# Kernel tuning notes

Hardware: AMD Instinct MI355X
Metric: run time of the kernel (lower is better)

## Reference

```python
import jax, jax.numpy as jnp
import numpy as np

HIDDEN = 2048
INTER = 4096
HEADS = 32
HEAD_DIM = INTER // HEADS  # 128
STATE = 128
GROUPS = 1
CONV_K = 4
CHUNK = 256
EPS = 1e-5
CONV_DIM = INTER + 2 * GROUPS * STATE  # 4352
DT_MIN, DT_MAX = 0.0, 100.0
BATCH, SEQ = 2, 4096


def _segment_sum(x):
    """Stable segment sum: returns (..., T, T) with entry [i,j] = sum_{k=j+1..i} x[k] (-inf above diag)."""
    T = x.shape[-1]
    xx = jnp.broadcast_to(x[..., None], x.shape + (T,))
    mask_lower = jnp.tril(jnp.ones((T, T), bool), -1)
    xx = jnp.where(mask_lower, xx, 0.0)
    seg = jnp.cumsum(xx, axis=-2)
    mask_incl = jnp.tril(jnp.ones((T, T), bool), 0)
    return jnp.where(mask_incl, seg, -jnp.inf)


def setup_inputs() -> dict:
    key = jax.random.key(0)
    ks = jax.random.split(key, 8)
    std = 0.02
    return {
        "hidden_states": jax.random.normal(ks[0], (BATCH, SEQ, HIDDEN), jnp.float32),
        "in_proj_w": jax.random.normal(ks[1], (INTER + CONV_DIM + HEADS, HIDDEN), jnp.float32) * std,
        "conv_w": jax.random.normal(ks[2], (CONV_DIM, 1, CONV_K), jnp.float32) * std,
        "conv_b": jnp.zeros((CONV_DIM,), jnp.float32),
        "A_log": jnp.log(jax.random.uniform(ks[3], (HEADS,), jnp.float32, 1.0, 16.0)),
        "dt_bias": jax.random.normal(ks[4], (HEADS,), jnp.float32) * 0.1,
        "D": jnp.ones((HEADS,), jnp.float32),
        "norm_w": jnp.ones((INTER,), jnp.float32),
        "out_proj_w": jax.random.normal(ks[5], (HIDDEN, INTER), jnp.float32) * (std / np.sqrt(48.0)),
    }


def reference(hidden_states, in_proj_w, conv_w, conv_b, A_log, dt_bias, D, norm_w, out_proj_w):
    b, s, _ = hidden_states.shape
    # in_proj and split into gate / conv-input / dt
    proj = hidden_states @ in_proj_w.T
    gate, hBC, dt = jnp.split(proj, [INTER, INTER + CONV_DIM], axis=-1)

    # causal depthwise conv1d (padding k-1 left, truncate to seq_len) + SiLU
    x = jnp.transpose(hBC, (0, 2, 1))  # (b, conv_dim, s)
    x = jax.lax.conv_general_dilated(
        x, conv_w, window_strides=(1,), padding=[(CONV_K - 1, 0)],
        dimension_numbers=("NCH", "OIH", "NCH"), feature_group_count=CONV_DIM)
    x = x + conv_b[None, :, None]
    hBC = jax.nn.silu(jnp.transpose(x, (0, 2, 1)))  # (b, s, conv_dim)

    xs, B, C = jnp.split(hBC, [INTER, INTER + GROUPS * STATE], axis=-1)

    A = -jnp.exp(A_log)  # (h,)
    dt = jnp.clip(jax.nn.softplus(dt + dt_bias), DT_MIN, DT_MAX)  # (b, s, h)

    xs = xs.reshape(b, s, HEADS, HEAD_DIM)
    rep = HEADS // GROUPS
    Bm = jnp.repeat(B.reshape(b, s, GROUPS, STATE), rep, axis=2)  # (b,s,h,n)
    Cm = jnp.repeat(C.reshape(b, s, GROUPS, STATE), rep, axis=2)

    pad = (-s) % CHUNK

    def padseq(t):
        return jnp.pad(t, ((0, 0), (0, pad)) + ((0, 0),) * (t.ndim - 2))

    D_res = D[None, None, :, None] * padseq(xs)  # (b, S, h, p)
    xdt = padseq(xs * dt[..., None])
    Ad = padseq(A[None, None, :] * dt)  # (b, S, h)
    Bm, Cm = padseq(Bm), padseq(Cm)

    nc = (s + pad) // CHUNK
    xdt = xdt.reshape(b, nc, CHUNK, HEADS, HEAD_DIM)
    Ad = jnp.transpose(Ad.reshape(b, nc, CHUNK, HEADS), (0, 3, 1, 2))  # (b,h,c,l)
    Bm = Bm.reshape(b, nc, CHUNK, HEADS, STATE)
    Cm = Cm.reshape(b, nc, CHUNK, HEADS, STATE)

    A_cum = jnp.cumsum(Ad, axis=-1)  # (b,h,c,l)

    # 1) intra-chunk (diagonal block) output
    L = jnp.exp(_segment_sum(Ad))  # (b,h,c,l,l)
    G = jnp.einsum("bclhn,bcshn->bclsh", Cm, Bm)
    M = G * jnp.transpose(L, (0, 2, 3, 4, 1))
    Y_diag = jnp.einsum("bclsh,bcshp->bclhp", M, xdt)

    # 2) per-chunk final states
    decay_states = jnp.exp(A_cum[:, :, :, -1:] - A_cum)  # (b,h,c,l)
    B_decay = Bm * jnp.transpose(decay_states, (0, 2, 3, 1))[..., None]
    states = jnp.einsum("bclhn,bclhp->bchpn", B_decay, xdt)  # (b,c,h,p,n)

    # 3) inter-chunk recurrence
    states = jnp.concatenate([jnp.zeros_like(states[:, :1]), states], axis=1)  # (b,c+1,h,p,n)
    chunk_sums = jnp.pad(A_cum[:, :, :, -1], ((0, 0), (0, 0), (1, 0)))  # (b,h,c+1)
    decay_chunk = jnp.exp(_segment_sum(chunk_sums))  # (b,h,c+1,c+1)
    decay_chunk = jnp.transpose(decay_chunk, (0, 2, 3, 1))  # (b,c,z,h)
    new_states = jnp.einsum("bczh,bchpn->bzhpn", decay_chunk, states)
    states = new_states[:, :-1]  # (b,c,h,p,n) state entering each chunk

    # 4) state -> output contribution
    state_decay = jnp.exp(A_cum)  # (b,h,c,l)
    Y_off = jnp.einsum("bclhn,bchpn->bclhp", Cm, states) * jnp.transpose(state_decay, (0, 2, 3, 1))[..., None]

    y = (Y_diag + Y_off).reshape(b, nc * CHUNK, HEADS, HEAD_DIM) + D_res
    y = y[:, :s].reshape(b, s, INTER)

    # gated RMSNorm
    y = y * jax.nn.silu(gate)
    var = jnp.mean(y * y, axis=-1, keepdims=True)
    y = y * jax.lax.rsqrt(var + EPS) * norm_w

    return y @ out_proj_w.T
```

## Files before the change

### kernel.cpp

```cpp
#include <hip/hip_runtime.h>

#define SEQ     4096
#define BATCH   2
#define NROWS   8192
#define HID     2048
#define INTER_  4096
#define NHEADS  32
#define HDIM    128
#define NSTATE  128
#define CDIM    4352
#define NPROJ_  8480
#define NPAD    8704
#define NCH     16
#define CHUNK_  256

typedef __attribute__((ext_vector_type(8))) short bf16x8;
typedef __attribute__((ext_vector_type(4))) short short4v;
typedef __attribute__((ext_vector_type(4))) float f32x4;

#define AS1 __attribute__((address_space(1)))
#define AS3 __attribute__((address_space(3)))

__device__ __forceinline__ float bf2f(short s) {
  union { unsigned u; float f; } x;
  x.u = ((unsigned)(unsigned short)s) << 16;
  return x.f;
}
__device__ __forceinline__ short f2bf(float f) {
  union { float f; unsigned u; } x; x.f = f;
  unsigned r = x.u + 0x7FFFu + ((x.u >> 16) & 1u);
  return (short)(r >> 16);
}

__global__ void cvt_bf16(const float* __restrict__ in, short* __restrict__ out,
                         int n4, int nsrc4) {
  int i = blockIdx.x * 256 + threadIdx.x;
  if (i >= n4) return;
  short4v o = {0, 0, 0, 0};
  if (i < nsrc4) {
    f32x4 v = *(const f32x4*)(in + (size_t)i * 4);
    o = (short4v){ f2bf(v.x), f2bf(v.y), f2bf(v.z), f2bf(v.w) };
  }
  *(short4v*)(out + (size_t)i * 4) = o;
}

template<int MODE>
__global__ __launch_bounds__(512, 1)
void gemm256(const short* __restrict__ A, const short* __restrict__ Bw,
             int M, int N, int K, int nM,
             float* __restrict__ outF, short* __restrict__ gate,
             short* __restrict__ hbc, float* __restrict__ dtraw)
{
  __shared__ __align__(16) short lds[2][2][2][256 * 32];
  const int tid = threadIdx.x;
  const int lane = tid & 63, wave = tid >> 6;
  const int l16 = lane & 15, lhi = lane >> 4;
  const int wm = wave >> 2, wn = wave & 3;

  const int bm = blockIdx.x % nM, bn = blockIdx.x / nM;
  const size_t row0 = (size_t)bm * 256;
  const int    col0 = bn * 256;

  const short* Ab  = A + row0 * K;
  const short* Bbp = Bw + (size_t)col0 * K;

  f32x4 acc[8][4];
  #pragma unroll
  for (int m = 0; m < 8; ++m)
    #pragma unroll
    for (int n = 0; n < 4; ++n) acc[m][n] = (f32x4){0.f, 0.f, 0.f, 0.f};

  auto stage = [&](int bufq, int mat, int kh, int ko) {
    const short* gsrc = mat ? Bbp : Ab;
    short* base = &lds[bufq][mat][kh][0];
    #pragma unroll
    for (int j = 0; j < 2; ++j) {
      int u = j * 512 + tid;
      int r = u >> 2;
      int g = (u & 3) ^ ((r >> 1) & 3);
      __builtin_amdgcn_global_load_lds(
          (const AS1 unsigned*)(gsrc + (size_t)r * K + ko + kh * 32 + g * 8),
          (AS3 unsigned*)(base + (j * 512 + wave * 64) * 8), 16, 0, 0);
    }
  };
  auto readA = [&](int bufq, int kh, int mh, bf16x8* a) {
    const short* base = &lds[bufq][0][kh][0];
    #pragma unroll
    for (int f = 0; f < 4; ++f) {
      int rr = wm * 128 + mh * 64 + f * 16 + l16;
      int g = lhi ^ ((rr >> 1) & 3);
      a[f] = *(const bf16x8*)(base + rr * 32 + g * 8);
    }
  };
  auto readB = [&](int bufq, int kh, bf16x8* b) {
    const short* base = &lds[bufq][1][kh][0];
    #pragma unroll
    for (int f = 0; f < 4; ++f) {
      int rr = wn * 64 + f * 16 + l16;
      int g = lhi ^ ((rr >> 1) & 3);
      b[f] = *(const bf16x8*)(base + rr * 32 + g * 8);
    }
  };

  const int nt = K / 64;
  stage(0, 0, 0, 0); stage(0, 1, 0, 0); stage(0, 0, 1, 0); stage(0, 1, 1, 0);
  asm volatile("s_waitcnt vmcnt(4)" ::: "memory");
  __builtin_amdgcn_s_barrier();

  for (int t = 0; t < nt; ++t) {
    const int buf = t & 1, nb = buf ^ 1;
    const int kon = (t + 1) * 64;
    const bool pf = (t + 1 < nt);

    #pragma unroll
    for (int kh = 0; kh < 2; ++kh) {
      if (pf) { stage(nb, 0, kh, kon); stage(nb, 1, kh, kon); }
      bf16x8 a[8], b[4];
      readA(buf, kh, 0, a); readA(buf, kh, 1, a + 4); readB(buf, kh, b);
      __builtin_amdgcn_s_setprio(1);
      #pragma unroll
      for (int mf = 0; mf < 8; ++mf)
        #pragma unroll
        for (int nf = 0; nf < 4; ++nf)
          acc[mf][nf] = __builtin_amdgcn_mfma_f32_16x16x32_bf16(a[mf], b[nf], acc[mf][nf], 0, 0, 0);
      __builtin_amdgcn_s_setprio(0);
      if (pf || kh == 0) {
        if (pf) asm volatile("s_waitcnt vmcnt(4)" ::: "memory");
        else    asm volatile("s_waitcnt vmcnt(0)" ::: "memory");
        __builtin_amdgcn_s_barrier();
      }
    }
  }

  #pragma unroll
  for (int mh = 0; mh < 2; ++mh) {
    #pragma unroll
    for (int f = 0; f < 4; ++f) {
      #pragma unroll
      for (int nf = 0; nf < 4; ++nf) {
        #pragma unroll
        for (int jq = 0; jq < 4; ++jq) {
          int gr = (int)row0 + wm * 128 + mh * 64 + f * 16 + lhi * 4 + jq;
          int gc = col0 + wn * 64 + nf * 16 + l16;
          float v = acc[mh * 4 + f][nf][jq];
          if (MODE == 0) {
            outF[(size_t)gr * N + gc] = v;
          } else {
            if (gc < INTER_)             gate[(size_t)gr * INTER_ + gc] = f2bf(v);
            else if (gc < INTER_ + CDIM) hbc[(size_t)gr * CDIM + (gc - INTER_)] = f2bf(v);
            else if (gc < NPROJ_)        dtraw[(size_t)gr * NHEADS + (gc - INTER_ - CDIM)] = v;
          }
        }
      }
    }
  }
}

__global__ __launch_bounds__(256)
void conv_t(const short* __restrict__ hbc, const float* __restrict__ cw,
            const float* __restrict__ cb, short* __restrict__ xsT,
            short* __restrict__ Bb, short* __restrict__ Cb, short* __restrict__ BbT)
{
  __shared__ short sOut[64][130];
  int ct = blockIdx.y;
  int cl = threadIdx.x & 127;
  int rh = threadIdx.x >> 7;
  int c = ct * 128 + cl;
  int row0 = blockIdx.x * 64;
  int s0 = row0 & (SEQ - 1);
  float w0 = cw[c * 4 + 0], w1 = cw[c * 4 + 1], w2 = cw[c * 4 + 2], w3 = cw[c * 4 + 3];
  float bias = cb[c];
  int r0 = rh * 32;
  float h0, h1, h2;
  h0 = (s0 + r0 - 3 >= 0) ? bf2f(hbc[(size_t)(row0 + r0 - 3) * CDIM + c]) : 0.f;
  h1 = (s0 + r0 - 2 >= 0) ? bf2f(hbc[(size_t)(row0 + r0 - 2) * CDIM + c]) : 0.f;
  h2 = (s0 + r0 - 1 >= 0) ? bf2f(hbc[(size_t)(row0 + r0 - 1) * CDIM + c]) : 0.f;

  for (int r = r0; r < r0 + 32; ++r) {
    float xin = bf2f(hbc[(size_t)(row0 + r) * CDIM + c]);
    float a = bias + w0 * h0 + w1 * h1 + w2 * h2 + w3 * xin;
    h0 = h1; h1 = h2; h2 = xin;
    float v = a / (1.f + expf(-a));
    short bv = f2bf(v);
    if (ct < 33) sOut[r][cl] = bv;
    if (ct == 32)      Bb[(size_t)(row0 + r) * NSTATE + cl] = bv;
    else if (ct == 33) Cb[(size_t)(row0 + r) * NSTATE + cl] = bv;
  }
  if (ct >= 33) return;
  __syncthreads();
  int p = threadIdx.x >> 1, sh = (threadIdx.x & 1) * 32;
  int b = row0 >> 12;
  size_t dst;
  short* outp;
  if (ct < 32) { outp = xsT; dst = ((size_t)(b * 32 + ct) * 128 + p) * SEQ + s0 + sh; }
  else         { outp = BbT; dst = ((size_t)b * 128 + p) * SEQ + s0 + sh; }
  #pragma unroll
  for (int g = 0; g < 8; ++g) {
    short4v o;
    o[0] = sOut[sh + g * 4 + 0][p];
    o[1] = sOut[sh + g * 4 + 1][p];
    o[2] = sOut[sh + g * 4 + 2][p];
    o[3] = sOut[sh + g * 4 + 3][p];
    *(short4v*)(outp + dst + g * 4) = o;
  }
}

__global__ void dt_proc(const float* __restrict__ dtraw, const float* __restrict__ dtb,
                        float* __restrict__ dtT, int n) {
  int i = blockIdx.x * 256 + threadIdx.x;
  if (i >= n) return;
  float x = dtraw[i] + dtb[i & (NHEADS - 1)];
  float sp = (x > 20.f) ? x : log1pf(expf(x));
  float d = fminf(fmaxf(sp, 0.f), 100.f);
  int row = i >> 5, h = i & 31;
  dtT[(size_t)h * NROWS + row] = d;
}

__global__ __launch_bounds__(256)
void ssm_state(const short* __restrict__ xsT, const short* __restrict__ BbT,
               const float* __restrict__ dtT, const float* __restrict__ Alog,
               short* __restrict__ csb, float* __restrict__ dAsum)
{
  int blk = blockIdx.x;
  int h = blk & 31, cc = (blk >> 5) & 15, b = blk >> 9;
  int tid = threadIdx.x, lane = tid & 63, wave = tid >> 6;
  int l16 = lane & 15, lhi = lane >> 4;
  int s0 = cc * CHUNK_;

  __shared__ float acum[256];
  __shared__ float sdt[256];
  __shared__ float wsum[4];
  { float Ah = -expf(Alog[h]);
    float d = dtT[(size_t)h * NROWS + (size_t)b * SEQ + s0 + tid];
    sdt[tid] = d;
    float v = Ah * d;
    #pragma unroll
    for (int off = 1; off < 64; off <<= 1) {
      float t = __shfl_up(v, off, 64);
      if (lane >= off) v += t;
    }
    if (lane == 63) wsum[wave] = v;
    __syncthreads();
    float addv = 0.f;
    #pragma unroll
    for (int w = 0; w < 3; ++w) if (w < wave) addv += wsum[w];
    acum[tid] = v + addv;
  }
  __syncthreads();
  float alast = acum[255];

  const short* xbase = xsT + ((size_t)(b * 32 + h) * 128) * SEQ + s0;
  const short* bbase = BbT + ((size_t)b * 128) * SEQ + s0;

  f32x4 acc[2][8];
  #pragma unroll
  for (int m = 0; m < 2; ++m)
    #pragma unroll
    for (int n = 0; n < 8; ++n) acc[m][n] = (f32x4){0.f, 0.f, 0.f, 0.f};

  for (int lt0 = 0; lt0 < 256; lt0 += 32) {
    float fe[8];
    #pragma unroll
    for (int e = 0; e < 8; ++e) {
      int kl = lt0 + lhi * 8 + e;
      fe[e] = sdt[kl] * __expf(alast - acum[kl]);
    }
    bf16x8 af[2];
    #pragma unroll
    for (int m = 0; m < 2; ++m) {
      bf16x8 raw = *(const bf16x8*)(xbase + (size_t)(wave * 32 + m * 16 + l16) * SEQ + lt0 + lhi * 8);
      bf16x8 sc;
      #pragma unroll
      for (int e = 0; e < 8; ++e) sc[e] = f2bf(bf2f(raw[e]) * fe[e]);
      af[m] = sc;
    }
    #pragma unroll
    for (int n = 0; n < 8; ++n) {
      bf16x8 bfv = *(const bf16x8*)(bbase + (size_t)(n * 16 + l16) * SEQ + lt0 + lhi * 8);
      acc[0][n] = __builtin_amdgcn_mfma_f32_16x16x32_bf16(af[0], bfv, acc[0][n], 0, 0, 0);
      acc[1][n] = __builtin_amdgcn_mfma_f32_16x16x32_bf16(af[1], bfv, acc[1][n], 0, 0, 0);
    }
  }
  size_t base = (size_t)blk * 16384;
  #pragma unroll
  for (int m = 0; m < 2; ++m)
    #pragma unroll
    for (int n = 0; n < 8; ++n)
      #pragma unroll
      for (int j = 0; j < 4; ++j) {
        int p = wave * 32 + m * 16 + lhi * 4 + j;
        int ng = n * 16 + l16;
        csb[base + (size_t)p * NSTATE + ng] = f2bf(acc[m][n][j]);
      }
  if (tid == 0) dAsum[blk] = alast;
}

__global__ void ssm_scan(short* __restrict__ csb, const float* __restrict__ dAsum) {
  int idx = blockIdx.x * 256 + threadIdx.x;
  int np = idx & 16383;
  int bh = idx >> 14;
  int h = bh & 31, b = bh >> 5;
  float run = 0.f;
  #pragma unroll
  for (int c = 0; c < NCH; ++c) {
    size_t base = ((size_t)((b * NCH + c) * NHEADS + h)) * 16384 + np;
    float v = bf2f(csb[base]);
    csb[base] = f2bf(run);
    run = run * __expf(dAsum[(b * NCH + c) * NHEADS + h]) + v;
  }
}

__global__ __launch_bounds__(256)
void ssm_y(const short* __restrict__ xsT, const short* __restrict__ Bb,
           const short* __restrict__ Cb, const float* __restrict__ dtT,
           const float* __restrict__ Alog, const float* __restrict__ Dv,
           const short* __restrict__ csb, short* __restrict__ gateY)
{
  int blk = blockIdx.y, lt = blockIdx.x;
  int h = blk & 31, cc = (blk >> 5) & 15, b = blk >> 9;
  int tid = threadIdx.x, lane = tid & 63, wave = tid >> 6;
  int l16 = lane & 15, lhi = lane >> 4;
  int s0 = cc * CHUNK_;
  size_t row0 = (size_t)b * SEQ + s0;

  __shared__ float acum[256];
  __shared__ float sdt[256];
  __shared__ float wsum[4];
  __shared__ __align__(16) short M_lds[64 * 264];

  { float Ah = -expf(Alog[h]);
    float d = dtT[(size_t)h * NROWS + row0 + tid];
    sdt[tid] = d;
    float v = Ah * d;
    #pragma unroll
    for (int off = 1; off < 64; off <<= 1) {
      float t = __shfl_up(v, off, 64);
      if (lane >= off) v += t;
    }
    if (lane == 63) wsum[wave] = v;
    __syncthreads();
    float addv = 0.f;
    #pragma unroll
    for (int w = 0; w < 3; ++w) if (w < wave) addv += wsum[w];
    acum[tid] = v + addv;
  }
  __syncthreads();

  float Dh = Dv[h];

  {
    f32x4 acc1[4][4];
    #pragma unroll
    for (int m = 0; m < 4; ++m)
      #pragma unroll
      for (int n = 0; n < 4; ++n) acc1[m][n] = (f32x4){0.f, 0.f, 0.f, 0.f};
    for (int kk = 0; kk < NSTATE; kk += 32) {
      bf16x8 af[4], bv[4];
      #pragma unroll
      for (int m = 0; m < 4; ++m)
        af[m] = *(const bf16x8*)(Cb + (row0 + lt * 64 + m * 16 + l16) * NSTATE + kk + lhi * 8);
      #pragma unroll
      for (int n = 0; n < 4; ++n)
        bv[n] = *(const bf16x8*)(Bb + (row0 + wave * 64 + n * 16 + l16) * NSTATE + kk + lhi * 8);
      #pragma unroll
      for (int m = 0; m < 4; ++m)
        #pragma unroll
        for (int n = 0; n < 4; ++n)
          acc1[m][n] = __builtin_amdgcn_mfma_f32_16x16x32_bf16(af[m], bv[n], acc1[m][n], 0, 0, 0);
    }
    float as_[4]; int sg_[4];
    #pragma unroll
    for (int n = 0; n < 4; ++n) { sg_[n] = wave * 64 + n * 16 + l16; as_[n] = acum[sg_[n]]; }
    #pragma unroll
    for (int m = 0; m < 4; ++m) {
      #pragma unroll
      for (int j = 0; j < 4; ++j) {
        int ll = m * 16 + lhi * 4 + j;
        int lg = lt * 64 + ll;
        float al = acum[lg];
        float dinv = Dh / fmaxf(sdt[lg], 1e-20f);
        #pragma unroll
        for (int n = 0; n < 4; ++n) {
          float v = 0.f;
          if (sg_[n] <= lg) {
            v = acc1[m][n][j] * __expf(al - as_[n]);
            if (sg_[n] == lg) v += dinv;
          }
          M_lds[ll * 264 + wave * 64 + n * 16 + l16] = f2bf(v);
        }
      }
    }
  }
  __syncthreads();

  const short* xbase = xsT + ((size_t)(b * 32 + h) * 128) * SEQ + s0;

  f32x4 accY[4][2];
  #pragma unroll
  for (int m = 0; m < 4; ++m) { accY[m][0] = (f32x4){0,0,0,0}; accY[m][1] = (f32x4){0,0,0,0}; }
  int smax = (lt + 1) * 64;
  for (int st = 0; st < smax; st += 32) {
    float fe[8];
    #pragma unroll
    for (int e = 0; e < 8; ++e) fe[e] = sdt[st + lhi * 8 + e];
    bf16x8 bv2[2];
    #pragma unroll
    for (int n = 0; n < 2; ++n) {
      bf16x8 raw = *(const bf16x8*)(xbase + (size_t)(wave * 32 + n * 16 + l16) * SEQ + st + lhi * 8);
      bf16x8 sc;
      #pragma unroll
      for (int e = 0; e < 8; ++e) sc[e] = f2bf(bf2f(raw[e]) * fe[e]);
      bv2[n] = sc;
    }
    #pragma unroll
    for (int m = 0; m < 4; ++m) {
      bf16x8 a = *(const bf16x8*)(M_lds + (m * 16 + l16) * 264 + st + lhi * 8);
      accY[m][0] = __builtin_amdgcn_mfma_f32_16x16x32_bf16(a, bv2[0], accY[m][0], 0, 0, 0);
      accY[m][1] = __builtin_amdgcn_mfma_f32_16x16x32_bf16(a, bv2[1], accY[m][1], 0, 0, 0);
    }
  }

  f32x4 accO[4][2];
  #pragma unroll
  for (int m = 0; m < 4; ++m) { accO[m][0] = (f32x4){0,0,0,0}; accO[m][1] = (f32x4){0,0,0,0}; }
  const short* sbase = csb + (size_t)blk * 16384;
  for (int nt = 0; nt < NSTATE; nt += 32) {
    bf16x8 bv2[2];
    #pragma unroll
    for (int n = 0; n < 2; ++n) {
      int p = wave * 32 + n * 16 + l16;
      bv2[n] = *(const bf16x8*)(sbase + (size_t)p * NSTATE + nt + lhi * 8);
    }
    #pragma unroll
    for (int m = 0; m < 4; ++m) {
      bf16x8 a = *(const bf16x8*)(Cb + (row0 + lt * 64 + m * 16 + l16) * NSTATE + nt + lhi * 8);
      accO[m][0] = __builtin_amdgcn_mfma_f32_16x16x32_bf16(a, bv2[0], accO[m][0], 0, 0, 0);
      accO[m][1] = __builtin_amdgcn_mfma_f32_16x16x32_bf16(a, bv2[1], accO[m][1], 0, 0, 0);
    }
  }

  #pragma unroll
  for (int m = 0; m < 4; ++m) {
    #pragma unroll
    for (int j = 0; j < 4; ++j) {
      int ll = m * 16 + lhi * 4 + j;
      float e = __expf(acum[lt * 64 + ll]);
      size_t row = row0 + lt * 64 + ll;
      #pragma unroll
      for (int n = 0; n < 2; ++n) {
        int p = wave * 32 + n * 16 + l16;
        size_t adr = row * INTER_ + h * HDIM + p;
        float yv = accY[m][n][j] + e * accO[m][n][j];
        float g = bf2f(gateY[adr]);
        gateY[adr] = f2bf(yv * g / (1.f + expf(-g)));
      }
    }
  }
}

__global__ __launch_bounds__(256)
void gate_norm(short* __restrict__ ybf, const float* __restrict__ nw)
{
  int row = blockIdx.x;
  int tid = threadIdx.x;
  size_t base = (size_t)row * INTER_;
  float vals[16];
  float ss = 0.f;
  #pragma unroll
  for (int i = 0; i < 16; ++i) {
    int idx = tid + i * 256;
    float v = bf2f(ybf[base + idx]);
    vals[i] = v;
    ss += v * v;
  }
  #pragma unroll
  for (int off = 32; off > 0; off >>= 1) ss += __shfl_down(ss, off);
  __shared__ float ws4[4];
  if ((tid & 63) == 0) ws4[tid >> 6] = ss;
  __syncthreads();
  float tot = ws4[0] + ws4[1] + ws4[2] + ws4[3];
  float scale = rsqrtf(tot * (1.f / 4096.f) + 1e-5f);
  #pragma unroll
  for (int i = 0; i < 16; ++i) {
    int idx = tid + i * 256;
    ybf[base + idx] = f2bf(vals[i] * scale * nw[idx]);
  }
}

extern "C" void kernel_launch(void* const* d_in, const int* in_sizes, int n_in,
                              void* d_out, int out_size, void* d_ws, size_t ws_size,
                              hipStream_t stream)
{
  const float* Xf   = (const float*)d_in[0];
  const float* W1f  = (const float*)d_in[1];
  const float* cw   = (const float*)d_in[2];
  const float* cb   = (const float*)d_in[3];
  const float* Alog = (const float*)d_in[4];
  const float* dtb  = (const float*)d_in[5];
  const float* Dv   = (const float*)d_in[6];
  const float* nw   = (const float*)d_in[7];
  const float* W2f  = (const float*)d_in[8];
  float* outp = (float*)d_out;
  char* ws = (char*)d_ws;

  size_t off = 0;
  short* Xb  = (short*)(ws + off); off += (size_t)NROWS * HID * 2;
  short* W1b = (short*)(ws + off); off += (size_t)NPAD * HID * 2;
  short* xsT = (short*)ws;
  short* W2b = (short*)(ws + off); off += (size_t)HID * INTER_ * 2;
  short* gateY = (short*)(ws + off); off += (size_t)NROWS * INTER_ * 2;
  short* hbc  = (short*)(ws + off); off += (size_t)NROWS * CDIM * 2;
  float* dtv  = (float*)(ws + off); off += (size_t)NROWS * NHEADS * 4;
  float* dtT  = (float*)(ws + off); off += (size_t)NROWS * NHEADS * 4;
  short* Bb   = (short*)(ws + off); off += (size_t)NROWS * NSTATE * 2;
  short* Cb   = (short*)(ws + off); off += (size_t)NROWS * NSTATE * 2;
  short* BbT  = (short*)(ws + off); off += (size_t)NROWS * NSTATE * 2;
  float* dAs  = (float*)(ws + off); off += 4096;
  short* csb  = (short*)hbc;

  cvt_bf16<<<(NROWS * HID / 4 + 255) / 256, 256, 0, stream>>>(
      Xf, Xb, NROWS * HID / 4, NROWS * HID / 4);
  cvt_bf16<<<(NPAD * HID / 4 + 255) / 256, 256, 0, stream>>>(
      W1f, W1b, NPAD * HID / 4, NPROJ_ * HID / 4);
  cvt_bf16<<<(HID * INTER_ / 4 + 255) / 256, 256, 0, stream>>>(
      W2f, W2b, HID * INTER_ / 4, HID * INTER_ / 4);

  gemm256<1><<<(NROWS / 256) * (NPAD / 256), 512, 0, stream>>>(
      Xb, W1b, NROWS, NPROJ_, HID, NROWS / 256, nullptr, gateY, hbc, dtv);

  dt_proc<<<(NROWS * NHEADS) / 256, 256, 0, stream>>>(dtv, dtb, dtT, NROWS * NHEADS);
  conv_t<<<dim3(NROWS / 64, 34), 256, 0, stream>>>(hbc, cw, cb, xsT, Bb, Cb, BbT);

  ssm_state<<<BATCH * NCH * NHEADS, 256, 0, stream>>>(xsT, BbT, dtT, Alog, csb, dAs);
  ssm_scan<<<(BATCH * NHEADS * 16384) / 256, 256, 0, stream>>>(csb, dAs);
  ssm_y<<<dim3(4, BATCH * NCH * NHEADS), 256, 0, stream>>>(xsT, Bb, Cb, dtT, Alog, Dv, csb, gateY);

  gate_norm<<<NROWS, 256, 0, stream>>>(gateY, nw);

  gemm256<0><<<(NROWS / 256) * (HID / 256), 512, 0, stream>>>(
      gateY, W2b, NROWS, HID, INTER_, NROWS / 256, outp, nullptr, nullptr, nullptr);
}
```

Baseline: 837.6 us.

## Vectorize conv and gate-norm loads, skip masked upper-triangle CB tiles

The conv kernel now has each thread handle 8 channels by 4 rows, using 16-byte bf16x8 loads of hbc and vector stores into shared memory and into the B/C buffers. The intra-chunk C·B^T MFMA block is skipped for waves above the causal diagonal (wave > lt). The gate_norm kernel switches from strided scalar bf16 accesses to contiguous 16-element vector loads and stores per thread. Together these cut memory transaction counts and wasted matrix work, at the cost of redundant halo loads in the conv and more registers per thread.

New measurement: 791.2 us, median of 2. 1.06x faster.

```diff
diff --git a/kernel.cpp b/kernel.cpp
--- a/kernel.cpp
+++ b/kernel.cpp
@@ -161,34 +161,55 @@
             const float* __restrict__ cb, short* __restrict__ xsT,
             short* __restrict__ Bb, short* __restrict__ Cb, short* __restrict__ BbT)
 {
-  __shared__ short sOut[64][130];
+  __shared__ short sOut[64][132];
   int ct = blockIdx.y;
-  int cl = threadIdx.x & 127;
-  int rh = threadIdx.x >> 7;
-  int c = ct * 128 + cl;
+  int t = threadIdx.x;
+  int cg = (t & 15) * 8;
+  int rg = (t >> 4) * 4;
+  int c0 = ct * 128 + cg;
   int row0 = blockIdx.x * 64;
   int s0 = row0 & (SEQ - 1);
-  float w0 = cw[c * 4 + 0], w1 = cw[c * 4 + 1], w2 = cw[c * 4 + 2], w3 = cw[c * 4 + 3];
-  float bias = cb[c];
-  int r0 = rh * 32;
-  float h0, h1, h2;
-  h0 = (s0 + r0 - 3 >= 0) ? bf2f(hbc[(size_t)(row0 + r0 - 3) * CDIM + c]) : 0.f;
-  h1 = (s0 + r0 - 2 >= 0) ? bf2f(hbc[(size_t)(row0 + r0 - 2) * CDIM + c]) : 0.f;
-  h2 = (s0 + r0 - 1 >= 0) ? bf2f(hbc[(size_t)(row0 + r0 - 1) * CDIM + c]) : 0.f;
-
-  for (int r = r0; r < r0 + 32; ++r) {
-    float xin = bf2f(hbc[(size_t)(row0 + r) * CDIM + c]);
-    float a = bias + w0 * h0 + w1 * h1 + w2 * h2 + w3 * xin;
-    h0 = h1; h1 = h2; h2 = xin;
-    float v = a / (1.f + expf(-a));
-    short bv = f2bf(v);
-    if (ct < 33) sOut[r][cl] = bv;
-    if (ct == 32)      Bb[(size_t)(row0 + r) * NSTATE + cl] = bv;
-    else if (ct == 33) Cb[(size_t)(row0 + r) * NSTATE + cl] = bv;
+
+  float w[4][8], bias[8];
+  #pragma unroll
+  for (int ch = 0; ch < 8; ++ch) {
+    f32x4 wv = *(const f32x4*)(cw + (size_t)(c0 + ch) * 4);
+    w[0][ch] = wv.x; w[1][ch] = wv.y; w[2][ch] = wv.z; w[3][ch] = wv.w;
+    bias[ch] = cb[c0 + ch];
+  }
+  float in[7][8];
+  #pragma unroll
+  for (int j = 0; j < 7; ++j) {
+    int sp = s0 + rg + j - 3;
+    if (sp >= 0) {
+      bf16x8 v = *(const bf16x8*)(hbc + (size_t)(row0 + rg + j - 3) * CDIM + c0);
+      #pragma unroll
+      for (int ch = 0; ch < 8; ++ch) in[j][ch] = bf2f(v[ch]);
+    } else {
+      #pragma unroll
+      for (int ch = 0; ch < 8; ++ch) in[j][ch] = 0.f;
+    }
+  }
+  #pragma unroll
+  for (int r = 0; r < 4; ++r) {
+    bf16x8 o;
+    #pragma unroll
+    for (int ch = 0; ch < 8; ++ch) {
+      float a = bias[ch] + w[0][ch] * in[r][ch] + w[1][ch] * in[r + 1][ch]
+                         + w[2][ch] * in[r + 2][ch] + w[3][ch] * in[r + 3][ch];
+      float v = a / (1.f + expf(-a));
+      o[ch] = f2bf(v);
+    }
+    if (ct < 33) {
+      *(short4v*)(&sOut[rg + r][cg])     = (short4v){o[0], o[1], o[2], o[3]};
+      *(short4v*)(&sOut[rg + r][cg + 4]) = (short4v){o[4], o[5], o[6], o[7]};
+    }
+    if (ct == 32)      *(bf16x8*)(Bb + (size_t)(row0 + rg + r) * NSTATE + cg) = o;
+    else if (ct == 33) *(bf16x8*)(Cb + (size_t)(row0 + rg + r) * NSTATE + cg) = o;
   }
   if (ct >= 33) return;
   __syncthreads();
-  int p = threadIdx.x >> 1, sh = (threadIdx.x & 1) * 32;
+  int p = t >> 1, sh = (t & 1) * 32;
   int b = row0 >> 12;
   size_t dst;
   short* outp;
@@ -348,7 +369,7 @@
 
   float Dh = Dv[h];
 
-  {
+  if (wave <= lt) {
     f32x4 acc1[4][4];
     #pragma unroll
     for (int m = 0; m < 4; ++m)
@@ -463,16 +484,17 @@
 {
   int row = blockIdx.x;
   int tid = threadIdx.x;
-  size_t base = (size_t)row * INTER_;
+  size_t base = (size_t)row * INTER_ + (size_t)tid * 16;
+  bf16x8 v0 = *(const bf16x8*)(ybf + base);
+  bf16x8 v1 = *(const bf16x8*)(ybf + base + 8);
   float vals[16];
   float ss = 0.f;
   #pragma unroll
-  for (int i = 0; i < 16; ++i) {
-    int idx = tid + i * 256;
-    float v = bf2f(ybf[base + idx]);
-    vals[i] = v;
-    ss += v * v;
-  }
+  for (int i = 0; i < 8; ++i) {
+    vals[i] = bf2f(v0[i]); vals[8 + i] = bf2f(v1[i]);
+  }
+  #pragma unroll
+  for (int i = 0; i < 16; ++i) ss += vals[i] * vals[i];
   #pragma unroll
   for (int off = 32; off > 0; off >>= 1) ss += __shfl_down(ss, off);
   __shared__ float ws4[4];
@@ -480,11 +502,14 @@
   __syncthreads();
   float tot = ws4[0] + ws4[1] + ws4[2] + ws4[3];
   float scale = rsqrtf(tot * (1.f / 4096.f) + 1e-5f);
-  #pragma unroll
-  for (int i = 0; i < 16; ++i) {
-    int idx = tid + i * 256;
-    ybf[base + idx] = f2bf(vals[i] * scale * nw[idx]);
-  }
+  bf16x8 o0, o1;
+  #pragma unroll
+  for (int i = 0; i < 8; ++i) {
+    o0[i] = f2bf(vals[i] * scale * nw[tid * 16 + i]);
+    o1[i] = f2bf(vals[8 + i] * scale * nw[tid * 16 + 8 + i]);
+  }
+  *(bf16x8*)(ybf + base) = o0;
+  *(bf16x8*)(ybf + base + 8) = o1;
 }
 
 extern "C" void kernel_launch(void* const* d_in, const int* in_sizes, int n_in,
```
